# Optimization experiments

Hardware: AMD Instinct MI355X
Metric: run time of the kernel (lower is better)

Reference implementation:

```python
import jax, jax.numpy as jnp
import numpy as np

FEAT = 1024   # feat_dim
EMB = 64      # emb_dim
GROUP = 16    # group == fc_dim
DG = FEAT // GROUP  # 64, per-group query/key dim and conv out channels per group
R = 1024      # num_rois
N = 1024      # nongt_dim


def setup_inputs() -> dict:
    key = jax.random.key(0)
    ks = jax.random.split(key, 8)
    inp = {
        "position_embedding": jax.random.normal(ks[0], (R, N, EMB), dtype=jnp.float32),
        "roi_feat": jax.random.normal(ks[1], (R, FEAT), dtype=jnp.float32),
        # fc_q / fc_k: Linear(feat_dim, feat_dim)
        "Wq": jax.random.normal(ks[2], (FEAT, FEAT), dtype=jnp.float32) * 0.02,
        "bq": jnp.zeros((FEAT,), dtype=jnp.float32),
        "Wk": jax.random.normal(ks[3], (FEAT, FEAT), dtype=jnp.float32) * 0.02,
        "bk": jnp.zeros((FEAT,), dtype=jnp.float32),
        # fc_pos_feat: Linear(emb_dim, fc_dim=group)
        "Wp": jax.random.normal(ks[4], (GROUP, EMB), dtype=jnp.float32) * 0.1,
        "bp": jnp.zeros((GROUP,), dtype=jnp.float32),
        # conv_cat: Conv2d(group*feat_dim, feat_dim, k=1, groups=group)
        # per group g: in FEAT channels -> out DG channels. Shape [GROUP, DG, FEAT].
        "Wc": jax.random.normal(ks[5], (GROUP, DG, FEAT), dtype=jnp.float32) * 0.02,
        "bc": jnp.zeros((FEAT,), dtype=jnp.float32),
        "nongt_dim": N,
    }
    return inp


def reference(position_embedding, roi_feat, Wq, bq, Wk, bk, Wp, bp, Wc, bc, nongt_dim):
    scale = 1.0 / np.sqrt(float(DG))
    # fc_pos_feat + relu -> aff_weight [R, GROUP, N]
    pos_feat = jax.nn.relu(jnp.einsum("rne,ge->rng", position_embedding, Wp) + bp)
    aff_weight = jnp.transpose(pos_feat, (0, 2, 1))  # [R, GROUP, N]
    nongt = roi_feat[:nongt_dim]                     # [N, FEAT]
    q = (roi_feat @ Wq.T + bq).reshape(-1, GROUP, DG)   # [R, GROUP, DG]
    k = (nongt @ Wk.T + bk).reshape(-1, GROUP, DG)      # [N, GROUP, DG]
    # per-group QK^T with log position bias
    aff = jnp.einsum("rgd,ngd->rgn", q, k) * scale      # [R, GROUP, N]
    weighted = jnp.log(jnp.clip(aff_weight, 1e-6, None)) + aff
    att = jax.nn.softmax(weighted, axis=2)              # [R, GROUP, N]
    # attention * V -> [R, GROUP, FEAT]
    out_t = jnp.einsum("rgn,nf->rgf", att, nongt)
    # grouped 1x1 conv combine: group g maps FEAT -> DG output channels
    out = jnp.einsum("rgf,gof->rgo", out_t, Wc).reshape(-1, FEAT) + bc
    return out
```

## Files before the change

kernel.cpp:

```cpp
#include <hip/hip_runtime.h>

#define R_DIM 1024
#define N_DIM 1024
#define FEAT  1024
#define EMB   64
#define GROUP 16
#define DG    64

typedef _Float16 half8  __attribute__((ext_vector_type(8)));
typedef _Float16 half4v __attribute__((ext_vector_type(4)));
typedef float    f32x4  __attribute__((ext_vector_type(4)));

__device__ __forceinline__ half8 cvt8(const float* p) {
  const float4 a = *(const float4*)p;
  const float4 b = *(const float4*)(p + 4);
  half8 h;
  h[0] = (_Float16)a.x; h[1] = (_Float16)a.y; h[2] = (_Float16)a.z; h[3] = (_Float16)a.w;
  h[4] = (_Float16)b.x; h[5] = (_Float16)b.y; h[6] = (_Float16)b.z; h[7] = (_Float16)b.w;
  return h;
}
__device__ __forceinline__ half8 cvt8v(float4 a, float4 b) {
  half8 h;
  h[0] = (_Float16)a.x; h[1] = (_Float16)a.y; h[2] = (_Float16)a.z; h[3] = (_Float16)a.w;
  h[4] = (_Float16)b.x; h[5] = (_Float16)b.y; h[6] = (_Float16)b.z; h[7] = (_Float16)b.w;
  return h;
}

__global__ __launch_bounds__(256) void qk_gemm(
    const float* __restrict__ roi, const float* __restrict__ Wq,
    const float* __restrict__ bq,  const float* __restrict__ Wk,
    const float* __restrict__ bk,  _Float16* __restrict__ qhI,
    _Float16* __restrict__ khI)
{
  __shared__ float aT[16][68];
  __shared__ float bqT[16][68];
  __shared__ float bkT[16][68];
  const int t  = threadIdx.x;
  const int r0 = blockIdx.x * 64, c0 = blockIdx.y * 64;
  const int lr = t >> 2, lk = (t & 3) << 2;
  const int ty = t >> 4, tx = t & 15;
  const float* ap  = roi + (r0 + lr) * FEAT + lk;
  const float* bqp = Wq  + (c0 + lr) * FEAT + lk;
  const float* bkp = Wk  + (c0 + lr) * FEAT + lk;
  float4 av  = *(const float4*)ap;
  float4 bqv = *(const float4*)bqp;
  float4 bkv = *(const float4*)bkp;
  float accq[4][4] = {}, acck[4][4] = {};
  for (int k0 = 0; k0 < FEAT; k0 += 16) {
    aT[lk+0][lr]=av.x;   aT[lk+1][lr]=av.y;   aT[lk+2][lr]=av.z;   aT[lk+3][lr]=av.w;
    bqT[lk+0][lr]=bqv.x; bqT[lk+1][lr]=bqv.y; bqT[lk+2][lr]=bqv.z; bqT[lk+3][lr]=bqv.w;
    bkT[lk+0][lr]=bkv.x; bkT[lk+1][lr]=bkv.y; bkT[lk+2][lr]=bkv.z; bkT[lk+3][lr]=bkv.w;
    __syncthreads();
    const bool more = (k0 + 16) < FEAT;
    float4 av_n, bqv_n, bkv_n;
    if (more) {
      av_n  = *(const float4*)(ap  + k0 + 16);
      bqv_n = *(const float4*)(bqp + k0 + 16);
      bkv_n = *(const float4*)(bkp + k0 + 16);
    }
#pragma unroll
    for (int kk = 0; kk < 16; ++kk) {
      const float4 a4 = *(const float4*)&aT[kk][ty << 2];
      const float4 q4 = *(const float4*)&bqT[kk][tx << 2];
      const float4 k4 = *(const float4*)&bkT[kk][tx << 2];
      const float ar[4] = {a4.x, a4.y, a4.z, a4.w};
      const float qr[4] = {q4.x, q4.y, q4.z, q4.w};
      const float kr[4] = {k4.x, k4.y, k4.z, k4.w};
#pragma unroll
      for (int i = 0; i < 4; ++i)
#pragma unroll
        for (int j = 0; j < 4; ++j) {
          accq[i][j] += ar[i] * qr[j];
          acck[i][j] += ar[i] * kr[j];
        }
    }
    __syncthreads();
    if (more) { av = av_n; bqv = bqv_n; bkv = bkv_n; }
  }
  const float4 bq4 = *(const float4*)(bq + c0 + (tx << 2));
  const float4 bk4 = *(const float4*)(bk + c0 + (tx << 2));
  const float bqr[4] = {bq4.x, bq4.y, bq4.z, bq4.w};
  const float bkr[4] = {bk4.x, bk4.y, bk4.z, bk4.w};
  const int g = c0 >> 6;
#pragma unroll
  for (int i = 0; i < 4; ++i) {
    half4v oq, ok;
#pragma unroll
    for (int j = 0; j < 4; ++j) {
      oq[j] = (_Float16)(accq[i][j] + bqr[j]);
      ok[j] = (_Float16)(acck[i][j] + bkr[j]);
    }
    const int row = r0 + (ty << 2) + i;
    const size_t idx = ((((size_t)g << 3) + (tx >> 1)) << 13) + ((size_t)row << 3) + ((tx & 1) << 2);
    *(half4v*)(qhI + idx) = oq;
    *(half4v*)(khI + idx) = ok;
  }
}

__global__ __launch_bounds__(256, 2) void pos_mfma(
    const float* __restrict__ pe, const float* __restrict__ Wp,
    const float* __restrict__ bp, _Float16* __restrict__ logw)
{
  __shared__ __align__(16) _Float16 SW[4][16][72];
  const int t = threadIdx.x;
  const int w = t >> 6, l = t & 63, q16 = l & 15, q4 = l >> 4;
  const float* wpp = Wp + (q16 << 6) + (q4 << 3);
  const half8 wb0 = cvt8(wpp);
  const half8 wb1 = cvt8(wpp + 32);
  const float bpg = bp[q16];

  const int tile0 = (blockIdx.x << 4) + (w << 2);
  const float* src = pe + ((size_t)tile0 << 10) + (q16 << 6) + (q4 << 3);

  float4 c[16];
#pragma unroll
  for (int it = 0; it < 4; ++it) {
    const float* s = src + ((size_t)it << 10);
    c[it * 4 + 0] = *(const float4*)(s);
    c[it * 4 + 1] = *(const float4*)(s + 4);
    c[it * 4 + 2] = *(const float4*)(s + 32);
    c[it * 4 + 3] = *(const float4*)(s + 36);
  }
  __builtin_amdgcn_sched_barrier(0);

#pragma unroll
  for (int it = 0; it < 4; ++it) {
    const half8 a0 = cvt8v(c[it * 4 + 0], c[it * 4 + 1]);
    const half8 a1 = cvt8v(c[it * 4 + 2], c[it * 4 + 3]);
    f32x4 acc = (f32x4){0.f, 0.f, 0.f, 0.f};
    acc = __builtin_amdgcn_mfma_f32_16x16x32_f16(a0, wb0, acc, 0, 0, 0);
    acc = __builtin_amdgcn_mfma_f32_16x16x32_f16(a1, wb1, acc, 0, 0, 0);
    half4v o;
#pragma unroll
    for (int j = 0; j < 4; ++j)
      o[j] = (_Float16)__logf(fmaxf(acc[j] + bpg, 1e-6f));
    *(half4v*)&SW[w][q16][(it << 4) + (q4 << 2)] = o;
  }
  __builtin_amdgcn_s_waitcnt(0);
  const int gg = l >> 2, cc = l & 3;
  const int r  = tile0 >> 6;
  const int n0 = ((tile0 & 63) << 4) + (cc << 4);
  _Float16* dst = logw + ((((size_t)r << 4) + gg) << 10) + n0;
  const half8 v0 = *(const half8*)&SW[w][gg][cc << 4];
  const half8 v1 = *(const half8*)&SW[w][gg][(cc << 4) + 8];
  *(half8*)(dst)     = v0;
  *(half8*)(dst + 8) = v1;
}

__global__ __launch_bounds__(256) void kc_gemm(
    const float* __restrict__ roi, const float* __restrict__ Wc,
    _Float16* __restrict__ kctI)
{
  __shared__ float aT[16][68];
  __shared__ float bT[16][68];
  const int t   = threadIdx.x;
  const int n0g = blockIdx.x * 64;
  const int g   = blockIdx.y;
  const int lr = t >> 2, lk = (t & 3) << 2;
  const int ty = t >> 4, tx = t & 15;
  const float* ap  = Wc  + (size_t)(g * DG + lr) * FEAT + lk;
  const float* bp_ = roi + (size_t)(n0g + lr) * FEAT + lk;
  float4 av = *(const float4*)ap;
  float4 bv = *(const float4*)bp_;
  float acc[4][4] = {};
  for (int k0 = 0; k0 < FEAT; k0 += 16) {
    aT[lk+0][lr]=av.x; aT[lk+1][lr]=av.y; aT[lk+2][lr]=av.z; aT[lk+3][lr]=av.w;
    bT[lk+0][lr]=bv.x; bT[lk+1][lr]=bv.y; bT[lk+2][lr]=bv.z; bT[lk+3][lr]=bv.w;
    __syncthreads();
    const bool more = (k0 + 16) < FEAT;
    float4 av_n, bv_n;
    if (more) {
      av_n = *(const float4*)(ap  + k0 + 16);
      bv_n = *(const float4*)(bp_ + k0 + 16);
    }
#pragma unroll
    for (int kk = 0; kk < 16; ++kk) {
      const float4 a4 = *(const float4*)&aT[kk][ty << 2];
      const float4 b4 = *(const float4*)&bT[kk][tx << 2];
      const float ar[4] = {a4.x, a4.y, a4.z, a4.w};
      const float br[4] = {b4.x, b4.y, b4.z, b4.w};
#pragma unroll
      for (int i = 0; i < 4; ++i)
#pragma unroll
        for (int j = 0; j < 4; ++j) acc[i][j] += ar[i] * br[j];
    }
    __syncthreads();
    if (more) { av = av_n; bv = bv_n; }
  }
#pragma unroll
  for (int i = 0; i < 4; ++i) {
    half4v o4;
#pragma unroll
    for (int j = 0; j < 4; ++j) o4[j] = (_Float16)acc[i][j];
    *(half4v*)(kctI + ((((size_t)g << 7) + ((n0g + (tx << 2)) >> 3)) << 9)
               + (((ty << 2) + i) << 3) + ((tx & 1) << 2)) = o4;
  }
}

#define PLD 1032
__global__ __launch_bounds__(256) void attn_mfma(
    const _Float16* __restrict__ qhI, const _Float16* __restrict__ khI,
    const _Float16* __restrict__ logw, const _Float16* __restrict__ kctI,
    const float* __restrict__ bc, float* __restrict__ outp)
{
  __shared__ __align__(16) union ShMem {
    _Float16 P[16][PLD];
    float    Ored[4][16][68];
  } sh;
  __shared__ float redm[4][16];
  __shared__ float redl[4][16];

  const int t   = threadIdx.x;
  const int w   = t >> 6;
  const int l   = t & 63;
  const int q16 = l & 15;
  const int q4  = l >> 4;
  const int g   = blockIdx.y;
  const int r0  = blockIdx.x << 4;
  const int nbase = w << 8;

  const _Float16* kbase = khI  + ((size_t)g << 16);
  const _Float16* qbase = qhI  + ((size_t)g << 16);
  const _Float16* cbase = kctI + ((size_t)g << 16);

  const half8 b0 = *(const half8*)(qbase + ((size_t)q4 << 13) + ((r0 + q16) << 3));
  const half8 b1 = *(const half8*)(qbase + ((size_t)(4 + q4) << 13) + ((r0 + q16) << 3));

  f32x4 S[16];
#pragma unroll
  for (int i = 0; i < 16; ++i) S[i] = (f32x4){0.f, 0.f, 0.f, 0.f};
#pragma unroll
  for (int t16 = 0; t16 < 16; ++t16) {
    const int n = nbase + (t16 << 4) + q16;
    const half8 k0 = *(const half8*)(kbase + ((size_t)q4 << 13) + (n << 3));
    const half8 k1 = *(const half8*)(kbase + ((size_t)(4 + q4) << 13) + (n << 3));
    S[t16] = __builtin_amdgcn_mfma_f32_16x16x32_f16(k0, b0, S[t16], 0, 0, 0);
    S[t16] = __builtin_amdgcn_mfma_f32_16x16x32_f16(k1, b1, S[t16], 0, 0, 0);
  }
  const _Float16* lwp = logw + ((((size_t)(r0 + q16)) << 4) + (size_t)g) * 1024;
#pragma unroll
  for (int t16 = 0; t16 < 16; ++t16) {
    const half4v lw = *(const half4v*)(lwp + nbase + (t16 << 4) + (q4 << 2));
#pragma unroll
    for (int j = 0; j < 4; ++j)
      S[t16][j] = S[t16][j] * 0.125f + (float)lw[j];
  }

  float m = -1e30f;
#pragma unroll
  for (int t16 = 0; t16 < 16; ++t16)
#pragma unroll
    for (int j = 0; j < 4; ++j) m = fmaxf(m, S[t16][j]);
  m = fmaxf(m, __shfl_xor(m, 16));
  m = fmaxf(m, __shfl_xor(m, 32));
  if (q4 == 0) redm[w][q16] = m;
  __syncthreads();
  m = fmaxf(fmaxf(redm[0][q16], redm[1][q16]), fmaxf(redm[2][q16], redm[3][q16]));

  float ls = 0.f;
#pragma unroll
  for (int t16 = 0; t16 < 16; ++t16) {
    half4v pv;
#pragma unroll
    for (int j = 0; j < 4; ++j) {
      const float p = __expf(S[t16][j] - m);
      ls += p;
      pv[j] = (_Float16)p;
    }
    *(half4v*)&sh.P[q16][nbase + (t16 << 4) + (q4 << 2)] = pv;
  }
  ls += __shfl_xor(ls, 16);
  ls += __shfl_xor(ls, 32);
  if (q4 == 0) redl[w][q16] = ls;
  __syncthreads();

  f32x4 O[4];
#pragma unroll
  for (int ot = 0; ot < 4; ++ot) O[ot] = (f32x4){0.f, 0.f, 0.f, 0.f};
#pragma unroll
  for (int ks = 0; ks < 8; ++ks) {
    const int nk = nbase + (ks << 5) + (q4 << 3);
    const half8 pa = *(const half8*)&sh.P[q16][nk];
#pragma unroll
    for (int ot = 0; ot < 4; ++ot) {
      const half8 bfr = *(const half8*)(cbase + ((size_t)(nk >> 3) << 9) + (((ot << 4) + q16) << 3));
      O[ot] = __builtin_amdgcn_mfma_f32_16x16x32_f16(pa, bfr, O[ot], 0, 0, 0);
    }
  }
  __syncthreads();
#pragma unroll
  for (int ot = 0; ot < 4; ++ot)
#pragma unroll
    for (int j = 0; j < 4; ++j)
      sh.Ored[w][(q4 << 2) + j][(ot << 4) + q16] = O[ot][j];
  __syncthreads();

  const int r  = t >> 4;
  const int o0 = (t & 15) << 2;
  const float lsum = redl[0][r] + redl[1][r] + redl[2][r] + redl[3][r];
  const float inv  = 1.0f / lsum;
  float o[4];
#pragma unroll
  for (int c = 0; c < 4; ++c)
    o[c] = sh.Ored[0][r][o0 + c] + sh.Ored[1][r][o0 + c] + sh.Ored[2][r][o0 + c] + sh.Ored[3][r][o0 + c];
  const float4 bcv = *(const float4*)(bc + (g << 6) + o0);
  float4 res;
  res.x = o[0] * inv + bcv.x;
  res.y = o[1] * inv + bcv.y;
  res.z = o[2] * inv + bcv.z;
  res.w = o[3] * inv + bcv.w;
  *(float4*)(outp + (size_t)(r0 + r) * FEAT + (g << 6) + o0) = res;
}

extern "C" void kernel_launch(void* const* d_in, const int* in_sizes, int n_in,
                              void* d_out, int out_size, void* d_ws, size_t ws_size,
                              hipStream_t stream)
{
  const float* pe  = (const float*)d_in[0];
  const float* roi = (const float*)d_in[1];
  const float* Wq  = (const float*)d_in[2];
  const float* bq  = (const float*)d_in[3];
  const float* Wk  = (const float*)d_in[4];
  const float* bk  = (const float*)d_in[5];
  const float* Wp  = (const float*)d_in[6];
  const float* bp  = (const float*)d_in[7];
  const float* Wc  = (const float*)d_in[8];
  const float* bc  = (const float*)d_in[9];
  float* outp = (float*)d_out;

  char* ws = (char*)d_ws;
  _Float16* qhI  = (_Float16*)(ws);
  _Float16* khI  = (_Float16*)(ws + ((size_t)2 << 20));
  _Float16* kctI = (_Float16*)(ws + ((size_t)4 << 20));
  _Float16* logw = (_Float16*)(ws + ((size_t)6 << 20));

  qk_gemm<<<dim3(16, 16), 256, 0, stream>>>(roi, Wq, bq, Wk, bk, qhI, khI);
  pos_mfma<<<4096, 256, 0, stream>>>(pe, Wp, bp, logw);
  kc_gemm<<<dim3(16, 16), 256, 0, stream>>>(roi, Wc, kctI);
  attn_mfma<<<dim3(64, 16), 256, 0, stream>>>(qhI, khI, logw, kctI, bc, outp);
}
```

Measured before the change: 190.8 us.

## Stream position embedding with nontemporal double-buffered loads and direct logw stores

In the position-feature kernel, all 16 float4 loads are no longer issued up front. It now loads one tile at a time with nontemporal loads and prefetches the next tile while computing the current one. The LDS transpose is dropped: each lane writes its 4-half log-weight chunk straight to global memory, and the occupancy hint in launch_bounds is removed. The aim is lower register pressure and less cache pollution on the large streaming read. The cost is narrower 8-byte global stores instead of 16-byte coalesced ones.

```diff
diff --git a/kernel.cpp b/kernel.cpp
--- a/kernel.cpp
+++ b/kernel.cpp
@@ -19,11 +19,14 @@
   h[4] = (_Float16)b.x; h[5] = (_Float16)b.y; h[6] = (_Float16)b.z; h[7] = (_Float16)b.w;
   return h;
 }
-__device__ __forceinline__ half8 cvt8v(float4 a, float4 b) {
+__device__ __forceinline__ half8 cvt8x(f32x4 a, f32x4 b) {
   half8 h;
-  h[0] = (_Float16)a.x; h[1] = (_Float16)a.y; h[2] = (_Float16)a.z; h[3] = (_Float16)a.w;
-  h[4] = (_Float16)b.x; h[5] = (_Float16)b.y; h[6] = (_Float16)b.z; h[7] = (_Float16)b.w;
+  h[0] = (_Float16)a[0]; h[1] = (_Float16)a[1]; h[2] = (_Float16)a[2]; h[3] = (_Float16)a[3];
+  h[4] = (_Float16)b[0]; h[5] = (_Float16)b[1]; h[6] = (_Float16)b[2]; h[7] = (_Float16)b[3];
   return h;
+}
+__device__ __forceinline__ f32x4 ntld(const float* p) {
+  return __builtin_nontemporal_load((const f32x4*)p);
 }
 
 __global__ __launch_bounds__(256) void qk_gemm(
@@ -97,11 +100,10 @@
   }
 }
 
-__global__ __launch_bounds__(256, 2) void pos_mfma(
+__global__ __launch_bounds__(256) void pos_mfma(
     const float* __restrict__ pe, const float* __restrict__ Wp,
     const float* __restrict__ bp, _Float16* __restrict__ logw)
 {
-  __shared__ __align__(16) _Float16 SW[4][16][72];
   const int t = threadIdx.x;
   const int w = t >> 6, l = t & 63, q16 = l & 15, q4 = l >> 4;
   const float* wpp = Wp + (q16 << 6) + (q4 << 3);
@@ -109,24 +111,26 @@
   const half8 wb1 = cvt8(wpp + 32);
   const float bpg = bp[q16];
 
-  const int tile0 = (blockIdx.x << 4) + (w << 2);
+  const int tile0 = ((blockIdx.x << 2) + w) << 2;
   const float* src = pe + ((size_t)tile0 << 10) + (q16 << 6) + (q4 << 3);
 
-  float4 c[16];
+  f32x4 c0 = ntld(src);
+  f32x4 c1 = ntld(src + 4);
+  f32x4 c2 = ntld(src + 32);
+  f32x4 c3 = ntld(src + 36);
 #pragma unroll
   for (int it = 0; it < 4; ++it) {
-    const float* s = src + ((size_t)it << 10);
-    c[it * 4 + 0] = *(const float4*)(s);
-    c[it * 4 + 1] = *(const float4*)(s + 4);
-    c[it * 4 + 2] = *(const float4*)(s + 32);
-    c[it * 4 + 3] = *(const float4*)(s + 36);
-  }
-  __builtin_amdgcn_sched_barrier(0);
-
-#pragma unroll
-  for (int it = 0; it < 4; ++it) {
-    const half8 a0 = cvt8v(c[it * 4 + 0], c[it * 4 + 1]);
-    const half8 a1 = cvt8v(c[it * 4 + 2], c[it * 4 + 3]);
+    f32x4 n0, n1, n2, n3;
+    if (it < 3) {
+      const float* s2 = src + ((size_t)(it + 1) << 10);
+      n0 = ntld(s2);
+      n1 = ntld(s2 + 4);
+      n2 = ntld(s2 + 32);
+      n3 = ntld(s2 + 36);
+    }
+    __builtin_amdgcn_sched_barrier(0);
+    const half8 a0 = cvt8x(c0, c1);
+    const half8 a1 = cvt8x(c2, c3);
     f32x4 acc = (f32x4){0.f, 0.f, 0.f, 0.f};
     acc = __builtin_amdgcn_mfma_f32_16x16x32_f16(a0, wb0, acc, 0, 0, 0);
     acc = __builtin_amdgcn_mfma_f32_16x16x32_f16(a1, wb1, acc, 0, 0, 0);
@@ -134,17 +138,12 @@
 #pragma unroll
     for (int j = 0; j < 4; ++j)
       o[j] = (_Float16)__logf(fmaxf(acc[j] + bpg, 1e-6f));
-    *(half4v*)&SW[w][q16][(it << 4) + (q4 << 2)] = o;
-  }
-  __builtin_amdgcn_s_waitcnt(0);
-  const int gg = l >> 2, cc = l & 3;
-  const int r  = tile0 >> 6;
-  const int n0 = ((tile0 & 63) << 4) + (cc << 4);
-  _Float16* dst = logw + ((((size_t)r << 4) + gg) << 10) + n0;
-  const half8 v0 = *(const half8*)&SW[w][gg][cc << 4];
-  const half8 v1 = *(const half8*)&SW[w][gg][(cc << 4) + 8];
-  *(half8*)(dst)     = v0;
-  *(half8*)(dst + 8) = v1;
+    const int tt = tile0 + it;
+    const int r  = tt >> 6;
+    const int nb = ((tt & 63) << 4) + (q4 << 2);
+    *(half4v*)(logw + ((((size_t)r << 4) + q16) << 10) + nb) = o;
+    if (it < 3) { c0 = n0; c1 = n1; c2 = n2; c3 = n3; }
+  }
 }
 
 __global__ __launch_bounds__(256) void kc_gemm(
```

Measured after the change: 202.4 us. +6.1%, slower.

## Merge three producer kernels into one block-dispatched launch

Applied to the files above, without the earlier changes.

Combines the Q/K projection GEMM, the Wc·roi GEMM and the position-embedding MFMA kernel into a single launch whose blocks branch on block index, with shared memory unioned across roles. The goal is to cut launch overhead and let the small, compute-bound GEMMs overlap with the bandwidth-bound position-embedding pass instead of running back to back. It also raises the attention kernel's launch_bounds minimum to 4 blocks per SM, which may limit registers. Risks: the union enlarges LDS for the pos-embedding blocks, which can lower their occupancy, and the sched_barrier in the pos path was removed.

```diff
diff --git a/kernel.cpp b/kernel.cpp
--- a/kernel.cpp
+++ b/kernel.cpp
@@ -6,6 +6,7 @@
 #define EMB   64
 #define GROUP 16
 #define DG    64
+#define PLD   1032
 
 typedef _Float16 half8  __attribute__((ext_vector_type(8)));
 typedef _Float16 half4v __attribute__((ext_vector_type(4)));
@@ -19,186 +20,180 @@
   h[4] = (_Float16)b.x; h[5] = (_Float16)b.y; h[6] = (_Float16)b.z; h[7] = (_Float16)b.w;
   return h;
 }
-__device__ __forceinline__ half8 cvt8v(float4 a, float4 b) {
+__device__ __forceinline__ half8 cvt8x(f32x4 a, f32x4 b) {
   half8 h;
-  h[0] = (_Float16)a.x; h[1] = (_Float16)a.y; h[2] = (_Float16)a.z; h[3] = (_Float16)a.w;
-  h[4] = (_Float16)b.x; h[5] = (_Float16)b.y; h[6] = (_Float16)b.z; h[7] = (_Float16)b.w;
+  h[0] = (_Float16)a[0]; h[1] = (_Float16)a[1]; h[2] = (_Float16)a[2]; h[3] = (_Float16)a[3];
+  h[4] = (_Float16)b[0]; h[5] = (_Float16)b[1]; h[6] = (_Float16)b[2]; h[7] = (_Float16)b[3];
   return h;
 }
 
-__global__ __launch_bounds__(256) void qk_gemm(
-    const float* __restrict__ roi, const float* __restrict__ Wq,
-    const float* __restrict__ bq,  const float* __restrict__ Wk,
-    const float* __restrict__ bk,  _Float16* __restrict__ qhI,
-    _Float16* __restrict__ khI)
+union ProdSh {
+  struct { float aT[16][68]; float b0T[16][68]; float b1T[16][68]; } gm;
+  _Float16 SW[4][16][72];
+};
+
+__global__ __launch_bounds__(256) void producers(
+    const float* __restrict__ pe,  const float* __restrict__ roi,
+    const float* __restrict__ Wq,  const float* __restrict__ bq,
+    const float* __restrict__ Wk,  const float* __restrict__ bk,
+    const float* __restrict__ Wp,  const float* __restrict__ bp,
+    const float* __restrict__ Wc,
+    _Float16* __restrict__ qhI, _Float16* __restrict__ khI,
+    _Float16* __restrict__ kctI, _Float16* __restrict__ logw)
 {
-  __shared__ float aT[16][68];
-  __shared__ float bqT[16][68];
-  __shared__ float bkT[16][68];
+  __shared__ ProdSh sh;
+  const int bx = blockIdx.x;
   const int t  = threadIdx.x;
-  const int r0 = blockIdx.x * 64, c0 = blockIdx.y * 64;
-  const int lr = t >> 2, lk = (t & 3) << 2;
-  const int ty = t >> 4, tx = t & 15;
-  const float* ap  = roi + (r0 + lr) * FEAT + lk;
-  const float* bqp = Wq  + (c0 + lr) * FEAT + lk;
-  const float* bkp = Wk  + (c0 + lr) * FEAT + lk;
-  float4 av  = *(const float4*)ap;
-  float4 bqv = *(const float4*)bqp;
-  float4 bkv = *(const float4*)bkp;
-  float accq[4][4] = {}, acck[4][4] = {};
-  for (int k0 = 0; k0 < FEAT; k0 += 16) {
-    aT[lk+0][lr]=av.x;   aT[lk+1][lr]=av.y;   aT[lk+2][lr]=av.z;   aT[lk+3][lr]=av.w;
-    bqT[lk+0][lr]=bqv.x; bqT[lk+1][lr]=bqv.y; bqT[lk+2][lr]=bqv.z; bqT[lk+3][lr]=bqv.w;
-    bkT[lk+0][lr]=bkv.x; bkT[lk+1][lr]=bkv.y; bkT[lk+2][lr]=bkv.z; bkT[lk+3][lr]=bkv.w;
-    __syncthreads();
-    const bool more = (k0 + 16) < FEAT;
-    float4 av_n, bqv_n, bkv_n;
-    if (more) {
-      av_n  = *(const float4*)(ap  + k0 + 16);
-      bqv_n = *(const float4*)(bqp + k0 + 16);
-      bkv_n = *(const float4*)(bkp + k0 + 16);
-    }
-#pragma unroll
-    for (int kk = 0; kk < 16; ++kk) {
-      const float4 a4 = *(const float4*)&aT[kk][ty << 2];
-      const float4 q4 = *(const float4*)&bqT[kk][tx << 2];
-      const float4 k4 = *(const float4*)&bkT[kk][tx << 2];
-      const float ar[4] = {a4.x, a4.y, a4.z, a4.w};
-      const float qr[4] = {q4.x, q4.y, q4.z, q4.w};
-      const float kr[4] = {k4.x, k4.y, k4.z, k4.w};
-#pragma unroll
-      for (int i = 0; i < 4; ++i)
-#pragma unroll
-        for (int j = 0; j < 4; ++j) {
-          accq[i][j] += ar[i] * qr[j];
-          acck[i][j] += ar[i] * kr[j];
-        }
-    }
-    __syncthreads();
-    if (more) { av = av_n; bqv = bqv_n; bkv = bkv_n; }
-  }
-  const float4 bq4 = *(const float4*)(bq + c0 + (tx << 2));
-  const float4 bk4 = *(const float4*)(bk + c0 + (tx << 2));
-  const float bqr[4] = {bq4.x, bq4.y, bq4.z, bq4.w};
-  const float bkr[4] = {bk4.x, bk4.y, bk4.z, bk4.w};
-  const int g = c0 >> 6;
-#pragma unroll
-  for (int i = 0; i < 4; ++i) {
-    half4v oq, ok;
-#pragma unroll
-    for (int j = 0; j < 4; ++j) {
-      oq[j] = (_Float16)(accq[i][j] + bqr[j]);
-      ok[j] = (_Float16)(acck[i][j] + bkr[j]);
-    }
-    const int row = r0 + (ty << 2) + i;
-    const size_t idx = ((((size_t)g << 3) + (tx >> 1)) << 13) + ((size_t)row << 3) + ((tx & 1) << 2);
-    *(half4v*)(qhI + idx) = oq;
-    *(half4v*)(khI + idx) = ok;
-  }
-}
-
-__global__ __launch_bounds__(256, 2) void pos_mfma(
-    const float* __restrict__ pe, const float* __restrict__ Wp,
-    const float* __restrict__ bp, _Float16* __restrict__ logw)
-{
-  __shared__ __align__(16) _Float16 SW[4][16][72];
-  const int t = threadIdx.x;
-  const int w = t >> 6, l = t & 63, q16 = l & 15, q4 = l >> 4;
-  const float* wpp = Wp + (q16 << 6) + (q4 << 3);
-  const half8 wb0 = cvt8(wpp);
-  const half8 wb1 = cvt8(wpp + 32);
-  const float bpg = bp[q16];
-
-  const int tile0 = (blockIdx.x << 4) + (w << 2);
-  const float* src = pe + ((size_t)tile0 << 10) + (q16 << 6) + (q4 << 3);
-
-  float4 c[16];
-#pragma unroll
-  for (int it = 0; it < 4; ++it) {
-    const float* s = src + ((size_t)it << 10);
-    c[it * 4 + 0] = *(const float4*)(s);
-    c[it * 4 + 1] = *(const float4*)(s + 4);
-    c[it * 4 + 2] = *(const float4*)(s + 32);
-    c[it * 4 + 3] = *(const float4*)(s + 36);
-  }
-  __builtin_amdgcn_sched_barrier(0);
-
-#pragma unroll
-  for (int it = 0; it < 4; ++it) {
-    const half8 a0 = cvt8v(c[it * 4 + 0], c[it * 4 + 1]);
-    const half8 a1 = cvt8v(c[it * 4 + 2], c[it * 4 + 3]);
-    f32x4 acc = (f32x4){0.f, 0.f, 0.f, 0.f};
-    acc = __builtin_amdgcn_mfma_f32_16x16x32_f16(a0, wb0, acc, 0, 0, 0);
-    acc = __builtin_amdgcn_mfma_f32_16x16x32_f16(a1, wb1, acc, 0, 0, 0);
-    half4v o;
-#pragma unroll
-    for (int j = 0; j < 4; ++j)
-      o[j] = (_Float16)__logf(fmaxf(acc[j] + bpg, 1e-6f));
-    *(half4v*)&SW[w][q16][(it << 4) + (q4 << 2)] = o;
-  }
-  __builtin_amdgcn_s_waitcnt(0);
-  const int gg = l >> 2, cc = l & 3;
-  const int r  = tile0 >> 6;
-  const int n0 = ((tile0 & 63) << 4) + (cc << 4);
-  _Float16* dst = logw + ((((size_t)r << 4) + gg) << 10) + n0;
-  const half8 v0 = *(const half8*)&SW[w][gg][cc << 4];
-  const half8 v1 = *(const half8*)&SW[w][gg][(cc << 4) + 8];
-  *(half8*)(dst)     = v0;
-  *(half8*)(dst + 8) = v1;
-}
-
-__global__ __launch_bounds__(256) void kc_gemm(
-    const float* __restrict__ roi, const float* __restrict__ Wc,
-    _Float16* __restrict__ kctI)
-{
-  __shared__ float aT[16][68];
-  __shared__ float bT[16][68];
-  const int t   = threadIdx.x;
-  const int n0g = blockIdx.x * 64;
-  const int g   = blockIdx.y;
-  const int lr = t >> 2, lk = (t & 3) << 2;
-  const int ty = t >> 4, tx = t & 15;
-  const float* ap  = Wc  + (size_t)(g * DG + lr) * FEAT + lk;
-  const float* bp_ = roi + (size_t)(n0g + lr) * FEAT + lk;
-  float4 av = *(const float4*)ap;
-  float4 bv = *(const float4*)bp_;
-  float acc[4][4] = {};
-  for (int k0 = 0; k0 < FEAT; k0 += 16) {
-    aT[lk+0][lr]=av.x; aT[lk+1][lr]=av.y; aT[lk+2][lr]=av.z; aT[lk+3][lr]=av.w;
-    bT[lk+0][lr]=bv.x; bT[lk+1][lr]=bv.y; bT[lk+2][lr]=bv.z; bT[lk+3][lr]=bv.w;
-    __syncthreads();
-    const bool more = (k0 + 16) < FEAT;
-    float4 av_n, bv_n;
-    if (more) {
-      av_n = *(const float4*)(ap  + k0 + 16);
-      bv_n = *(const float4*)(bp_ + k0 + 16);
-    }
-#pragma unroll
-    for (int kk = 0; kk < 16; ++kk) {
-      const float4 a4 = *(const float4*)&aT[kk][ty << 2];
-      const float4 b4 = *(const float4*)&bT[kk][tx << 2];
-      const float ar[4] = {a4.x, a4.y, a4.z, a4.w};
-      const float br[4] = {b4.x, b4.y, b4.z, b4.w};
-#pragma unroll
-      for (int i = 0; i < 4; ++i)
-#pragma unroll
-        for (int j = 0; j < 4; ++j) acc[i][j] += ar[i] * br[j];
-    }
-    __syncthreads();
-    if (more) { av = av_n; bv = bv_n; }
-  }
-#pragma unroll
-  for (int i = 0; i < 4; ++i) {
-    half4v o4;
-#pragma unroll
-    for (int j = 0; j < 4; ++j) o4[j] = (_Float16)acc[i][j];
-    *(half4v*)(kctI + ((((size_t)g << 7) + ((n0g + (tx << 2)) >> 3)) << 9)
-               + (((ty << 2) + i) << 3) + ((tx & 1) << 2)) = o4;
-  }
-}
-
-#define PLD 1032
-__global__ __launch_bounds__(256) void attn_mfma(
+
+  if (bx < 256) {
+    const int r0 = (bx >> 4) << 6, c0 = (bx & 15) << 6;
+    const int lr = t >> 2, lk = (t & 3) << 2;
+    const int ty = t >> 4, tx = t & 15;
+    const float* ap  = roi + (r0 + lr) * FEAT + lk;
+    const float* bqp = Wq  + (c0 + lr) * FEAT + lk;
+    const float* bkp = Wk  + (c0 + lr) * FEAT + lk;
+    float4 av  = *(const float4*)ap;
+    float4 bqv = *(const float4*)bqp;
+    float4 bkv = *(const float4*)bkp;
+    float accq[4][4] = {}, acck[4][4] = {};
+    for (int k0 = 0; k0 < FEAT; k0 += 16) {
+      sh.gm.aT [lk+0][lr]=av.x;  sh.gm.aT [lk+1][lr]=av.y;  sh.gm.aT [lk+2][lr]=av.z;  sh.gm.aT [lk+3][lr]=av.w;
+      sh.gm.b0T[lk+0][lr]=bqv.x; sh.gm.b0T[lk+1][lr]=bqv.y; sh.gm.b0T[lk+2][lr]=bqv.z; sh.gm.b0T[lk+3][lr]=bqv.w;
+      sh.gm.b1T[lk+0][lr]=bkv.x; sh.gm.b1T[lk+1][lr]=bkv.y; sh.gm.b1T[lk+2][lr]=bkv.z; sh.gm.b1T[lk+3][lr]=bkv.w;
+      __syncthreads();
+      const bool more = (k0 + 16) < FEAT;
+      float4 av_n, bqv_n, bkv_n;
+      if (more) {
+        av_n  = *(const float4*)(ap  + k0 + 16);
+        bqv_n = *(const float4*)(bqp + k0 + 16);
+        bkv_n = *(const float4*)(bkp + k0 + 16);
+      }
+#pragma unroll
+      for (int kk = 0; kk < 16; ++kk) {
+        const float4 a4 = *(const float4*)&sh.gm.aT [kk][ty << 2];
+        const float4 q4 = *(const float4*)&sh.gm.b0T[kk][tx << 2];
+        const float4 k4 = *(const float4*)&sh.gm.b1T[kk][tx << 2];
+        const float ar[4] = {a4.x, a4.y, a4.z, a4.w};
+        const float qr[4] = {q4.x, q4.y, q4.z, q4.w};
+        const float kr[4] = {k4.x, k4.y, k4.z, k4.w};
+#pragma unroll
+        for (int i = 0; i < 4; ++i)
+#pragma unroll
+          for (int j = 0; j < 4; ++j) {
+            accq[i][j] += ar[i] * qr[j];
+            acck[i][j] += ar[i] * kr[j];
+          }
+      }
+      __syncthreads();
+      if (more) { av = av_n; bqv = bqv_n; bkv = bkv_n; }
+    }
+    const float4 bq4 = *(const float4*)(bq + c0 + (tx << 2));
+    const float4 bk4 = *(const float4*)(bk + c0 + (tx << 2));
+    const float bqr[4] = {bq4.x, bq4.y, bq4.z, bq4.w};
+    const float bkr[4] = {bk4.x, bk4.y, bk4.z, bk4.w};
+    const int g = c0 >> 6;
+#pragma unroll
+    for (int i = 0; i < 4; ++i) {
+      half4v oq, ok;
+#pragma unroll
+      for (int j = 0; j < 4; ++j) {
+        oq[j] = (_Float16)(accq[i][j] + bqr[j]);
+        ok[j] = (_Float16)(acck[i][j] + bkr[j]);
+      }
+      const int row = r0 + (ty << 2) + i;
+      const size_t idx = ((((size_t)g << 3) + (tx >> 1)) << 13) + ((size_t)row << 3) + ((tx & 1) << 2);
+      *(half4v*)(qhI + idx) = oq;
+      *(half4v*)(khI + idx) = ok;
+    }
+  } else if (bx < 512) {
+    const int k   = bx - 256;
+    const int g   = k >> 4;
+    const int n0g = (k & 15) << 6;
+    const int lr = t >> 2, lk = (t & 3) << 2;
+    const int ty = t >> 4, tx = t & 15;
+    const float* ap  = Wc  + (size_t)(g * DG + lr) * FEAT + lk;
+    const float* bp_ = roi + (size_t)(n0g + lr) * FEAT + lk;
+    float4 av = *(const float4*)ap;
+    float4 bv = *(const float4*)bp_;
+    float acc[4][4] = {};
+    for (int k0 = 0; k0 < FEAT; k0 += 16) {
+      sh.gm.aT [lk+0][lr]=av.x; sh.gm.aT [lk+1][lr]=av.y; sh.gm.aT [lk+2][lr]=av.z; sh.gm.aT [lk+3][lr]=av.w;
+      sh.gm.b0T[lk+0][lr]=bv.x; sh.gm.b0T[lk+1][lr]=bv.y; sh.gm.b0T[lk+2][lr]=bv.z; sh.gm.b0T[lk+3][lr]=bv.w;
+      __syncthreads();
+      const bool more = (k0 + 16) < FEAT;
+      float4 av_n, bv_n;
+      if (more) {
+        av_n = *(const float4*)(ap  + k0 + 16);
+        bv_n = *(const float4*)(bp_ + k0 + 16);
+      }
+#pragma unroll
+      for (int kk = 0; kk < 16; ++kk) {
+        const float4 a4 = *(const float4*)&sh.gm.aT [kk][ty << 2];
+        const float4 b4 = *(const float4*)&sh.gm.b0T[kk][tx << 2];
+        const float ar[4] = {a4.x, a4.y, a4.z, a4.w};
+        const float br[4] = {b4.x, b4.y, b4.z, b4.w};
+#pragma unroll
+        for (int i = 0; i < 4; ++i)
+#pragma unroll
+          for (int j = 0; j < 4; ++j) acc[i][j] += ar[i] * br[j];
+      }
+      __syncthreads();
+      if (more) { av = av_n; bv = bv_n; }
+    }
+#pragma unroll
+    for (int i = 0; i < 4; ++i) {
+      half4v o4;
+#pragma unroll
+      for (int j = 0; j < 4; ++j) o4[j] = (_Float16)acc[i][j];
+      *(half4v*)(kctI + ((((size_t)g << 7) + ((n0g + (tx << 2)) >> 3)) << 9)
+                 + (((ty << 2) + i) << 3) + ((tx & 1) << 2)) = o4;
+    }
+  } else {
+    const int p = bx - 512;
+    const int w = t >> 6, l = t & 63, q16 = l & 15, q4 = l >> 4;
+    const float* wpp = Wp + (q16 << 6) + (q4 << 3);
+    const half8 wb0 = cvt8(wpp);
+    const half8 wb1 = cvt8(wpp + 32);
+    const float bpg = bp[q16];
+
+    const int tile0 = (p << 4) + (w << 2);
+    const float* src = pe + ((size_t)tile0 << 10) + (q16 << 6) + (q4 << 3);
+
+    f32x4 c[16];
+#pragma unroll
+    for (int it = 0; it < 4; ++it) {
+      const float* s = src + ((size_t)it << 10);
+      c[it * 4 + 0] = *(const f32x4*)(s);
+      c[it * 4 + 1] = *(const f32x4*)(s + 4);
+      c[it * 4 + 2] = *(const f32x4*)(s + 32);
+      c[it * 4 + 3] = *(const f32x4*)(s + 36);
+    }
+#pragma unroll
+    for (int it = 0; it < 4; ++it) {
+      const half8 a0 = cvt8x(c[it * 4 + 0], c[it * 4 + 1]);
+      const half8 a1 = cvt8x(c[it * 4 + 2], c[it * 4 + 3]);
+      f32x4 acc = (f32x4){0.f, 0.f, 0.f, 0.f};
+      acc = __builtin_amdgcn_mfma_f32_16x16x32_f16(a0, wb0, acc, 0, 0, 0);
+      acc = __builtin_amdgcn_mfma_f32_16x16x32_f16(a1, wb1, acc, 0, 0, 0);
+      half4v o;
+#pragma unroll
+      for (int j = 0; j < 4; ++j)
+        o[j] = (_Float16)__logf(fmaxf(acc[j] + bpg, 1e-6f));
+      *(half4v*)&sh.SW[w][q16][(it << 4) + (q4 << 2)] = o;
+    }
+    __builtin_amdgcn_s_waitcnt(0);
+    const int gg = l >> 2, cc = l & 3;
+    const int r  = tile0 >> 6;
+    const int n0 = ((tile0 & 63) << 4) + (cc << 4);
+    _Float16* dst = logw + ((((size_t)r << 4) + gg) << 10) + n0;
+    const half8 v0 = *(const half8*)&sh.SW[w][gg][cc << 4];
+    const half8 v1 = *(const half8*)&sh.SW[w][gg][(cc << 4) + 8];
+    *(half8*)(dst)     = v0;
+    *(half8*)(dst + 8) = v1;
+  }
+}
+
+__global__ __launch_bounds__(256, 4) void attn_mfma(
     const _Float16* __restrict__ qhI, const _Float16* __restrict__ khI,
     const _Float16* __restrict__ logw, const _Float16* __restrict__ kctI,
     const float* __restrict__ bc, float* __restrict__ outp)
@@ -334,8 +329,7 @@
   _Float16* kctI = (_Float16*)(ws + ((size_t)4 << 20));
   _Float16* logw = (_Float16*)(ws + ((size_t)6 << 20));
 
-  qk_gemm<<<dim3(16, 16), 256, 0, stream>>>(roi, Wq, bq, Wk, bk, qhI, khI);
-  pos_mfma<<<4096, 256, 0, stream>>>(pe, Wp, bp, logw);
-  kc_gemm<<<dim3(16, 16), 256, 0, stream>>>(roi, Wc, kctI);
+  producers<<<4608, 256, 0, stream>>>(pe, roi, Wq, bq, Wk, bk, Wp, bp, Wc,
+                                      qhI, khI, kctI, logw);
   attn_mfma<<<dim3(64, 16), 256, 0, stream>>>(qhI, khI, logw, kctI, bc, outp);
 }
```

Result: slower. 206.4 us (+8.2%).
